# Kernel tuning notes

Measured on AMD Instinct MI355X. Metric: run time of the kernel, lower is better.

Reference implementation:

```python
import jax, jax.numpy as jnp
import numpy as np

BATCH = 2048
N = 2 * BATCH
TEMP = 0.5
BN_EPS = 1e-5
COS_EPS = 1e-8

# Precompute (constant) flat indices of the negative entries: all (i,j) with
# j != i and j != i +- BATCH. Each row has exactly N-2 negatives.
_mask = np.ones((N, N), dtype=bool)
np.fill_diagonal(_mask, False)
for _i in range(BATCH):
    _mask[_i, BATCH + _i] = False
    _mask[BATCH + _i, _i] = False
NEG_IDX = np.nonzero(_mask.reshape(-1))[0]  # (N*(N-2),)


def _projector(h, W1, gamma, beta, W2, b2):
    # Linear (no bias) -> BatchNorm1d (training-mode batch stats) -> ReLU -> Linear
    x = h @ W1.T                                   # (B, latent)
    mu = jnp.mean(x, axis=0)
    var = jnp.mean(jnp.square(x - mu), axis=0)     # biased var, as torch BN
    x = (x - mu) * jax.lax.rsqrt(var + BN_EPS) * gamma + beta
    x = jax.nn.relu(x)
    return x @ W2.T + b2                           # (B, proj)


def setup_inputs() -> dict:
    key = jax.random.key(0)
    ks = jax.random.split(key, 4)
    latent, proj = 2048, 256
    return {
        "h_i": jax.random.normal(ks[0], (BATCH, latent), jnp.float32),
        "h_j": jax.random.normal(ks[1], (BATCH, latent), jnp.float32),
        "W1": jax.random.normal(ks[2], (latent, latent), jnp.float32) / np.sqrt(latent),
        "gamma": jnp.ones((latent,), jnp.float32),
        "beta": jnp.zeros((latent,), jnp.float32),
        "W2": jax.random.normal(ks[3], (proj, latent), jnp.float32) / np.sqrt(latent),
        "b2": jnp.zeros((proj,), jnp.float32),
    }


def reference(h_i, h_j, W1, gamma, beta, W2, b2):
    z_i = _projector(h_i, W1, gamma, beta, W2, b2)
    z_j = _projector(h_j, W1, gamma, beta, W2, b2)
    z = jnp.concatenate([z_i, z_j], axis=0)                      # (N, proj)
    # cosine similarity: normalize once, then a single GEMM
    zn = z / jnp.maximum(jnp.linalg.norm(z, axis=1, keepdims=True), COS_EPS)
    sim = (zn @ zn.T) / TEMP                                     # (N, N)
    sim_i_j = jnp.diagonal(sim, offset=BATCH)                    # (BATCH,)
    sim_j_i = jnp.diagonal(sim, offset=-BATCH)                   # (BATCH,)
    positives = jnp.concatenate([sim_i_j, sim_j_i])[:, None]     # (N, 1)
    negatives = sim.reshape(-1)[NEG_IDX].reshape(N, N - 2)       # (N, N-2)
    logits = jnp.concatenate([positives, negatives], axis=1)     # (N, N-1)
    # cross-entropy with label 0 for every row, reduction='sum', then / N
    loss = jnp.sum(jax.nn.logsumexp(logits, axis=1) - logits[:, 0]) / N
    return loss
```

## Files before the change

### kernel.cpp

```cpp
#include <hip/hip_runtime.h>
#include <math.h>

#define BATCH   2048
#define NROWS   4096
#define LATENT  2048
#define PROJ    256
#define TEMP_INV 2.0f
#define BN_EPS  1e-5f
#define COS_EPS 1e-8f

typedef __bf16 bf16x8 __attribute__((ext_vector_type(8)));
typedef float  f32x4  __attribute__((ext_vector_type(4)));

__device__ __forceinline__ unsigned short f2bf(float f) {
    union { float f; unsigned int u; } c; c.f = f;
    return (unsigned short)((c.u + 0x7FFFu + ((c.u >> 16) & 1u)) >> 16);
}
__device__ __forceinline__ float bf2f(unsigned short h) {
    union { unsigned int u; float f; } c; c.u = ((unsigned int)h) << 16;
    return c.f;
}

__device__ __forceinline__ void gl_lds16(const unsigned short* g, unsigned short* l) {
    __builtin_amdgcn_global_load_lds(
        (__attribute__((address_space(1))) void*)g,
        (__attribute__((address_space(3))) void*)l, 16, 0, 0);
}

__device__ __forceinline__ int swz(int R, int lk) {
    return R * 32 + ((lk ^ ((R >> 1) & 3)) << 3);
}

#define G1 1048576
#define G2 2097152
#define G3 3145728
#define G4 3276800
__global__ __launch_bounds__(256) void cvt_all_kernel(
    const float* __restrict__ h_i, const float* __restrict__ h_j,
    const float* __restrict__ W1,  const float* __restrict__ W2,
    unsigned short* __restrict__ dst)
{
    int i = blockIdx.x * 256 + threadIdx.x;
    if (i >= G4) return;
    const float* src; int off;
    if (i < G1)      { src = h_i; off = i; }
    else if (i < G2) { src = h_j; off = i - G1; }
    else if (i < G3) { src = W1;  off = i - G2; }
    else             { src = W2;  off = i - G3; }
    float4 v = reinterpret_cast<const float4*>(src)[off];
    ushort4 o;
    o.x = f2bf(v.x); o.y = f2bf(v.y); o.z = f2bf(v.z); o.w = f2bf(v.w);
    reinterpret_cast<ushort4*>(dst)[i] = o;
}

template<int KSTRIDE, int KLEN, int WM, int WN>
__device__ __forceinline__ void mfma_loop(
    const unsigned short* __restrict__ Ab,
    const unsigned short* __restrict__ Bb,
    unsigned short* As, unsigned short* Bs,
    f32x4 acc[WM][WN], int tid)
{
    constexpr int BM = WM * 32;
    constexpr int BN = WN * 32;
    const int wid = tid >> 6, lane = tid & 63;
    const int mblk = (wid >> 1) * (WM * 16);
    const int nblk = (wid & 1) * (WN * 16);
    const int lr = lane & 15, lk = lane >> 4;
    for (int k0 = 0; k0 < KLEN; k0 += 32) {
        __syncthreads();
        #pragma unroll
        for (int u = 0; u < BM / 64; ++u) {
            int li = u * 256 + tid;
            int r = li >> 2;
            int c = (li & 3) ^ ((li >> 3) & 3);
            gl_lds16(Ab + (size_t)r * KSTRIDE + k0 + c * 8, As + li * 8);
        }
        #pragma unroll
        for (int u = 0; u < BN / 64; ++u) {
            int li = u * 256 + tid;
            int r = li >> 2;
            int c = (li & 3) ^ ((li >> 3) & 3);
            gl_lds16(Bb + (size_t)r * KSTRIDE + k0 + c * 8, Bs + li * 8);
        }
        __syncthreads();
        bf16x8 af[WM], bv[WN];
        #pragma unroll
        for (int i = 0; i < WM; ++i)
            af[i] = *reinterpret_cast<const bf16x8*>(As + swz(mblk + i * 16 + lr, lk));
        #pragma unroll
        for (int j = 0; j < WN; ++j)
            bv[j] = *reinterpret_cast<const bf16x8*>(Bs + swz(nblk + j * 16 + lr, lk));
        #pragma unroll
        for (int i = 0; i < WM; ++i)
            #pragma unroll
            for (int j = 0; j < WN; ++j)
                acc[i][j] = __builtin_amdgcn_mfma_f32_16x16x32_bf16(af[i], bv[j], acc[i][j], 0, 0, 0);
    }
}

__global__ __launch_bounds__(256) void gemm1_mfma(
    const unsigned short* __restrict__ Hb, const unsigned short* __restrict__ W1b,
    unsigned short* __restrict__ Xb, float* __restrict__ sums, float* __restrict__ sumsqs)
{
    __shared__ __align__(16) unsigned short As[128 * 32];
    __shared__ __align__(16) unsigned short Bs[128 * 32];
    const int tid = threadIdx.x;
    const int m0 = blockIdx.y * 128, n0 = blockIdx.x * 128;
    f32x4 zero = {0.f, 0.f, 0.f, 0.f};
    f32x4 acc[4][4];
    #pragma unroll
    for (int i = 0; i < 4; ++i)
        #pragma unroll
        for (int j = 0; j < 4; ++j) acc[i][j] = zero;
    mfma_loop<LATENT, LATENT, 4, 4>(Hb + (size_t)m0 * LATENT, W1b + (size_t)n0 * LATENT,
                                    As, Bs, acc, tid);
    const int wid = tid >> 6, lane = tid & 63;
    const int mblk = (wid >> 1) * 64, nblk = (wid & 1) * 64;
    const int lr = lane & 15, lq = lane >> 4;
    const int half = m0 >> 11;
    #pragma unroll
    for (int j = 0; j < 4; ++j) {
        float s = 0.f, q = 0.f;
        #pragma unroll
        for (int i = 0; i < 4; ++i)
            #pragma unroll
            for (int r = 0; r < 4; ++r) {
                float v = acc[i][j][r];
                s += v; q += v * v;
                int row = m0 + mblk + i * 16 + lq * 4 + r;
                int col = n0 + nblk + j * 16 + lr;
                Xb[(size_t)row * LATENT + col] = f2bf(v);
            }
        s += __shfl_xor(s, 16, 64);  q += __shfl_xor(q, 16, 64);
        s += __shfl_xor(s, 32, 64);  q += __shfl_xor(q, 32, 64);
        if (lq == 0) {
            int col = n0 + nblk + j * 16 + lr;
            atomicAdd(&sums[half * LATENT + col], s);
            atomicAdd(&sumsqs[half * LATENT + col], q);
        }
    }
}

__global__ __launch_bounds__(256) void bnrelu_kernel(
    unsigned short* __restrict__ Xb, const float* __restrict__ sums,
    const float* __restrict__ sumsqs, const float* __restrict__ gamma,
    const float* __restrict__ beta)
{
    const int row = blockIdx.x;
    const int half = row >> 11;
    const int col = threadIdx.x * 8;
    size_t idx = (size_t)row * LATENT + col;
    ushort4 a = *reinterpret_cast<const ushort4*>(Xb + idx);
    ushort4 b = *reinterpret_cast<const ushort4*>(Xb + idx + 4);
    const float* S = sums + half * LATENT + col;
    const float* Q = sumsqs + half * LATENT + col;
    float4 s0 = *reinterpret_cast<const float4*>(S);
    float4 s1 = *reinterpret_cast<const float4*>(S + 4);
    float4 q0 = *reinterpret_cast<const float4*>(Q);
    float4 q1 = *reinterpret_cast<const float4*>(Q + 4);
    float4 g0 = *reinterpret_cast<const float4*>(gamma + col);
    float4 g1 = *reinterpret_cast<const float4*>(gamma + col + 4);
    float4 e0 = *reinterpret_cast<const float4*>(beta + col);
    float4 e1 = *reinterpret_cast<const float4*>(beta + col + 4);
    ushort4 oa, ob;
    #define BN1(x, sv, qv, gv, ev, o) { \
        float mu = (sv) * (1.0f / BATCH); \
        float var = (qv) * (1.0f / BATCH) - mu * mu; \
        float sc = (gv) * rsqrtf(var + BN_EPS); \
        float sh = (ev) - mu * sc; \
        o = f2bf(fmaxf(fmaf(bf2f(x), sc, sh), 0.f)); }
    BN1(a.x, s0.x, q0.x, g0.x, e0.x, oa.x) BN1(a.y, s0.y, q0.y, g0.y, e0.y, oa.y)
    BN1(a.z, s0.z, q0.z, g0.z, e0.z, oa.z) BN1(a.w, s0.w, q0.w, g0.w, e0.w, oa.w)
    BN1(b.x, s1.x, q1.x, g1.x, e1.x, ob.x) BN1(b.y, s1.y, q1.y, g1.y, e1.y, ob.y)
    BN1(b.z, s1.z, q1.z, g1.z, e1.z, ob.z) BN1(b.w, s1.w, q1.w, g1.w, e1.w, ob.w)
    #undef BN1
    *reinterpret_cast<ushort4*>(Xb + idx) = oa;
    *reinterpret_cast<ushort4*>(Xb + idx + 4) = ob;
}

__global__ __launch_bounds__(256) void gemm2_mfma(
    const unsigned short* __restrict__ Xb, const unsigned short* __restrict__ W2b,
    float* __restrict__ Zp)
{
    __shared__ __align__(16) unsigned short As[128 * 32];
    __shared__ __align__(16) unsigned short Bs[64 * 32];
    const int tid = threadIdx.x;
    const int m0 = blockIdx.y * 128, n0 = blockIdx.x * 64, kc = blockIdx.z;
    f32x4 zero = {0.f, 0.f, 0.f, 0.f};
    f32x4 acc[4][2];
    #pragma unroll
    for (int i = 0; i < 4; ++i) { acc[i][0] = zero; acc[i][1] = zero; }
    mfma_loop<LATENT, 512, 4, 2>(Xb + (size_t)m0 * LATENT + kc * 512,
                                 W2b + (size_t)n0 * LATENT + kc * 512, As, Bs, acc, tid);
    float* Zk = Zp + (size_t)kc * NROWS * PROJ;
    const int wid = tid >> 6, lane = tid & 63;
    const int mblk = (wid >> 1) * 64, nblk = (wid & 1) * 32;
    const int lr = lane & 15, lq = lane >> 4;
    #pragma unroll
    for (int i = 0; i < 4; ++i)
        #pragma unroll
        for (int j = 0; j < 2; ++j)
            #pragma unroll
            for (int r = 0; r < 4; ++r) {
                int row = m0 + mblk + i * 16 + lq * 4 + r;
                int col = n0 + nblk + j * 16 + lr;
                Zk[(size_t)row * PROJ + col] = acc[i][j][r];
            }
}

__global__ __launch_bounds__(256) void rownorm_kernel(
    const float* __restrict__ Zp, const float* __restrict__ b2,
    unsigned short* __restrict__ ZNb)
{
    const int wave = threadIdx.x >> 6;
    const int lane = threadIdx.x & 63;
    const int row = blockIdx.x * 4 + wave;
    float v[4];
    float sq = 0.f;
    #pragma unroll
    for (int i = 0; i < 4; ++i) {
        int col = lane + i * 64;
        float t = b2[col];
        #pragma unroll
        for (int c = 0; c < 4; ++c)
            t += Zp[(size_t)c * NROWS * PROJ + (size_t)row * PROJ + col];
        v[i] = t;
        sq += t * t;
    }
    #pragma unroll
    for (int off = 32; off > 0; off >>= 1) sq += __shfl_xor(sq, off, 64);
    float inv = 1.0f / fmaxf(sqrtf(sq), COS_EPS);
    #pragma unroll
    for (int i = 0; i < 4; ++i)
        ZNb[(size_t)row * PROJ + lane + i * 64] = f2bf(v[i] * inv);
}

__global__ __launch_bounds__(256) void simlse_mfma(
    const unsigned short* __restrict__ ZNb, float* __restrict__ rowsum,
    float* __restrict__ dgA, float* __restrict__ posA)
{
    __shared__ __align__(16) unsigned short As[128 * 32];
    __shared__ __align__(16) unsigned short Bs[128 * 32];
    const int tid = threadIdx.x;
    const int r0 = blockIdx.y * 128, j0 = blockIdx.x * 128;
    f32x4 zero = {0.f, 0.f, 0.f, 0.f};
    f32x4 acc[4][4];
    #pragma unroll
    for (int i = 0; i < 4; ++i)
        #pragma unroll
        for (int j = 0; j < 4; ++j) acc[i][j] = zero;
    mfma_loop<PROJ, PROJ, 4, 4>(ZNb + (size_t)r0 * PROJ, ZNb + (size_t)j0 * PROJ,
                                As, Bs, acc, tid);
    const int wid = tid >> 6, lane = tid & 63;
    const int mblk = (wid >> 1) * 64, nblk = (wid & 1) * 64;
    const int lr = lane & 15, lq = lane >> 4;
    #pragma unroll
    for (int i = 0; i < 4; ++i)
        #pragma unroll
        for (int r = 0; r < 4; ++r) {
            int R = r0 + mblk + i * 16 + lq * 4 + r;
            int P = (R < BATCH) ? R + BATCH : R - BATCH;
            float t = 0.f;
            #pragma unroll
            for (int j = 0; j < 4; ++j) {
                int J = j0 + nblk + j * 16 + lr;
                float s = acc[i][j][r] * TEMP_INV;
                float e = __expf(s);
                t += e;
                if (J == R) dgA[R] = e;
                if (J == P) posA[R] = s;
            }
            t += __shfl_xor(t, 1, 64);
            t += __shfl_xor(t, 2, 64);
            t += __shfl_xor(t, 4, 64);
            t += __shfl_xor(t, 8, 64);
            if (lr == 0) atomicAdd(&rowsum[R], t);
        }
}

__global__ __launch_bounds__(256) void loss_kernel(
    const float* __restrict__ rowsum, const float* __restrict__ dgA,
    const float* __restrict__ posA, float* __restrict__ out)
{
    __shared__ float red[256];
    float s = 0.f;
    for (int r = threadIdx.x; r < NROWS; r += 256)
        s += logf(rowsum[r] - dgA[r]) - posA[r];
    red[threadIdx.x] = s;
    __syncthreads();
    for (int off = 128; off > 0; off >>= 1) {
        if (threadIdx.x < off) red[threadIdx.x] += red[threadIdx.x + off];
        __syncthreads();
    }
    if (threadIdx.x == 0) out[0] = red[0] * (1.0f / NROWS);
}

extern "C" void kernel_launch(void* const* d_in, const int* in_sizes, int n_in,
                              void* d_out, int out_size, void* d_ws, size_t ws_size,
                              hipStream_t stream)
{
    const float* h_i   = (const float*)d_in[0];
    const float* h_j   = (const float*)d_in[1];
    const float* W1    = (const float*)d_in[2];
    const float* gamma = (const float*)d_in[3];
    const float* beta  = (const float*)d_in[4];
    const float* W2    = (const float*)d_in[5];
    const float* b2    = (const float*)d_in[6];
    float* out = (float*)d_out;

    float* Zp     = (float*)d_ws;
    float* sums   = Zp + (size_t)4 * NROWS * PROJ;
    float* sumsqs = sums + 2 * LATENT;
    float* rowsum = sumsqs + 2 * LATENT;
    float* dgA    = rowsum + NROWS;
    float* posA   = dgA + NROWS;
    unsigned short* Hb  = (unsigned short*)(posA + NROWS);
    unsigned short* W1b = Hb + (size_t)NROWS * LATENT;
    unsigned short* W2b = W1b + (size_t)LATENT * LATENT;
    unsigned short* Xb  = W2b + (size_t)PROJ * LATENT;
    unsigned short* ZNb = Xb + (size_t)NROWS * LATENT;

    hipMemsetAsync(sums, 0, (size_t)(4 * LATENT + NROWS) * sizeof(float), stream);

    cvt_all_kernel<<<(G4 + 255) / 256, 256, 0, stream>>>(h_i, h_j, W1, W2, Hb);
    gemm1_mfma<<<dim3(LATENT / 128, NROWS / 128), 256, 0, stream>>>(Hb, W1b, Xb, sums, sumsqs);
    bnrelu_kernel<<<NROWS, 256, 0, stream>>>(Xb, sums, sumsqs, gamma, beta);
    gemm2_mfma<<<dim3(PROJ / 64, NROWS / 128, 4), 256, 0, stream>>>(Xb, W2b, Zp);
    rownorm_kernel<<<NROWS / 4, 256, 0, stream>>>(Zp, b2, ZNb);
    simlse_mfma<<<dim3(NROWS / 128, NROWS / 128), 256, 0, stream>>>(ZNb, rowsum, dgA, posA);
    loss_kernel<<<1, 256, 0, stream>>>(rowsum, dgA, posA, out);
}
```

Measured before the change: 204.7 us.

## Double-buffer LDS tiles in the shared MFMA GEMM loop

```diff
diff --git a/kernel.cpp b/kernel.cpp
--- a/kernel.cpp
+++ b/kernel.cpp
@@ -54,7 +54,7 @@
 }
 
 template<int KSTRIDE, int KLEN, int WM, int WN>
-__device__ __forceinline__ void mfma_loop(
+__device__ __forceinline__ void mfma_loop_db(
     const unsigned short* __restrict__ Ab,
     const unsigned short* __restrict__ Bb,
     unsigned short* As, unsigned short* Bs,
@@ -66,30 +66,48 @@
     const int mblk = (wid >> 1) * (WM * 16);
     const int nblk = (wid & 1) * (WN * 16);
     const int lr = lane & 15, lk = lane >> 4;
+
+    #pragma unroll
+    for (int u = 0; u < BM / 64; ++u) {
+        int li = u * 256 + tid;
+        int r = li >> 2, c = (li & 3) ^ ((li >> 3) & 3);
+        gl_lds16(Ab + (size_t)r * KSTRIDE + c * 8, As + li * 8);
+    }
+    #pragma unroll
+    for (int u = 0; u < BN / 64; ++u) {
+        int li = u * 256 + tid;
+        int r = li >> 2, c = (li & 3) ^ ((li >> 3) & 3);
+        gl_lds16(Bb + (size_t)r * KSTRIDE + c * 8, Bs + li * 8);
+    }
+
     for (int k0 = 0; k0 < KLEN; k0 += 32) {
+        const int cur = (k0 >> 5) & 1;
+        unsigned short* Ac = As + cur * (BM * 32);
+        unsigned short* Bc = Bs + cur * (BN * 32);
         __syncthreads();
-        #pragma unroll
-        for (int u = 0; u < BM / 64; ++u) {
-            int li = u * 256 + tid;
-            int r = li >> 2;
-            int c = (li & 3) ^ ((li >> 3) & 3);
-            gl_lds16(Ab + (size_t)r * KSTRIDE + k0 + c * 8, As + li * 8);
+        if (k0 + 32 < KLEN) {
+            unsigned short* An = As + (cur ^ 1) * (BM * 32);
+            unsigned short* Bn = Bs + (cur ^ 1) * (BN * 32);
+            #pragma unroll
+            for (int u = 0; u < BM / 64; ++u) {
+                int li = u * 256 + tid;
+                int r = li >> 2, c = (li & 3) ^ ((li >> 3) & 3);
+                gl_lds16(Ab + (size_t)r * KSTRIDE + k0 + 32 + c * 8, An + li * 8);
+            }
+            #pragma unroll
+            for (int u = 0; u < BN / 64; ++u) {
+                int li = u * 256 + tid;
+                int r = li >> 2, c = (li & 3) ^ ((li >> 3) & 3);
+                gl_lds16(Bb + (size_t)r * KSTRIDE + k0 + 32 + c * 8, Bn + li * 8);
+            }
         }
-        #pragma unroll
-        for (int u = 0; u < BN / 64; ++u) {
-            int li = u * 256 + tid;
-            int r = li >> 2;
-            int c = (li & 3) ^ ((li >> 3) & 3);
-            gl_lds16(Bb + (size_t)r * KSTRIDE + k0 + c * 8, Bs + li * 8);
-        }
-        __syncthreads();
         bf16x8 af[WM], bv[WN];
         #pragma unroll
         for (int i = 0; i < WM; ++i)
-            af[i] = *reinterpret_cast<const bf16x8*>(As + swz(mblk + i * 16 + lr, lk));
+            af[i] = *reinterpret_cast<const bf16x8*>(Ac + swz(mblk + i * 16 + lr, lk));
         #pragma unroll
         for (int j = 0; j < WN; ++j)
-            bv[j] = *reinterpret_cast<const bf16x8*>(Bs + swz(nblk + j * 16 + lr, lk));
+            bv[j] = *reinterpret_cast<const bf16x8*>(Bc + swz(nblk + j * 16 + lr, lk));
         #pragma unroll
         for (int i = 0; i < WM; ++i)
             #pragma unroll
@@ -102,8 +120,8 @@
     const unsigned short* __restrict__ Hb, const unsigned short* __restrict__ W1b,
     unsigned short* __restrict__ Xb, float* __restrict__ sums, float* __restrict__ sumsqs)
 {
-    __shared__ __align__(16) unsigned short As[128 * 32];
-    __shared__ __align__(16) unsigned short Bs[128 * 32];
+    __shared__ __align__(16) unsigned short As[2 * 128 * 32];
+    __shared__ __align__(16) unsigned short Bs[2 * 128 * 32];
     const int tid = threadIdx.x;
     const int m0 = blockIdx.y * 128, n0 = blockIdx.x * 128;
     f32x4 zero = {0.f, 0.f, 0.f, 0.f};
@@ -112,8 +130,8 @@
     for (int i = 0; i < 4; ++i)
         #pragma unroll
         for (int j = 0; j < 4; ++j) acc[i][j] = zero;
-    mfma_loop<LATENT, LATENT, 4, 4>(Hb + (size_t)m0 * LATENT, W1b + (size_t)n0 * LATENT,
-                                    As, Bs, acc, tid);
+    mfma_loop_db<LATENT, LATENT, 4, 4>(Hb + (size_t)m0 * LATENT, W1b + (size_t)n0 * LATENT,
+                                       As, Bs, acc, tid);
     const int wid = tid >> 6, lane = tid & 63;
     const int mblk = (wid >> 1) * 64, nblk = (wid & 1) * 64;
     const int lr = lane & 15, lq = lane >> 4;
@@ -182,16 +200,16 @@
     const unsigned short* __restrict__ Xb, const unsigned short* __restrict__ W2b,
     float* __restrict__ Zp)
 {
-    __shared__ __align__(16) unsigned short As[128 * 32];
-    __shared__ __align__(16) unsigned short Bs[64 * 32];
+    __shared__ __align__(16) unsigned short As[2 * 128 * 32];
+    __shared__ __align__(16) unsigned short Bs[2 * 64 * 32];
     const int tid = threadIdx.x;
     const int m0 = blockIdx.y * 128, n0 = blockIdx.x * 64, kc = blockIdx.z;
     f32x4 zero = {0.f, 0.f, 0.f, 0.f};
     f32x4 acc[4][2];
     #pragma unroll
     for (int i = 0; i < 4; ++i) { acc[i][0] = zero; acc[i][1] = zero; }
-    mfma_loop<LATENT, 512, 4, 2>(Xb + (size_t)m0 * LATENT + kc * 512,
-                                 W2b + (size_t)n0 * LATENT + kc * 512, As, Bs, acc, tid);
+    mfma_loop_db<LATENT, 512, 4, 2>(Xb + (size_t)m0 * LATENT + kc * 512,
+                                    W2b + (size_t)n0 * LATENT + kc * 512, As, Bs, acc, tid);
     float* Zk = Zp + (size_t)kc * NROWS * PROJ;
     const int wid = tid >> 6, lane = tid & 63;
     const int mblk = (wid >> 1) * 64, nblk = (wid & 1) * 32;
@@ -239,8 +257,8 @@
     const unsigned short* __restrict__ ZNb, float* __restrict__ rowsum,
     float* __restrict__ dgA, float* __restrict__ posA)
 {
-    __shared__ __align__(16) unsigned short As[128 * 32];
-    __shared__ __align__(16) unsigned short Bs[128 * 32];
+    __shared__ __align__(16) unsigned short As[2 * 128 * 32];
+    __shared__ __align__(16) unsigned short Bs[2 * 128 * 32];
     const int tid = threadIdx.x;
     const int r0 = blockIdx.y * 128, j0 = blockIdx.x * 128;
     f32x4 zero = {0.f, 0.f, 0.f, 0.f};
@@ -249,8 +267,8 @@
     for (int i = 0; i < 4; ++i)
         #pragma unroll
         for (int j = 0; j < 4; ++j) acc[i][j] = zero;
-    mfma_loop<PROJ, PROJ, 4, 4>(ZNb + (size_t)r0 * PROJ, ZNb + (size_t)j0 * PROJ,
-                                As, Bs, acc, tid);
+    mfma_loop_db<PROJ, PROJ, 4, 4>(ZNb + (size_t)r0 * PROJ, ZNb + (size_t)j0 * PROJ,
+                                   As, Bs, acc, tid);
     const int wid = tid >> 6, lane = tid & 63;
     const int mblk = (wid >> 1) * 64, nblk = (wid & 1) * 64;
     const int lr = lane & 15, lq = lane >> 4;
```

Result: slower. 214.2 us (+4.6%).
